# Performance work log

Hardware: AMD Instinct MI355X
Metric: run time of the kernel (lower is better)

The kernel has to match this reference:

```python
import jax, jax.numpy as jnp
import numpy as np

N = 100000   # nodes
E = 1600000  # edges (avg degree 16)
D = 64       # feature / hidden / embedding dim
OUT = 2
NEG_SLOPE = 0.2


def setup_inputs() -> dict:
    key = jax.random.key(0)
    ks = jax.random.split(key, 12)
    s = 1.0 / np.sqrt(D)
    return {
        "x": jax.random.normal(ks[0], (N, D), dtype=jnp.float32),
        "edge_index": jax.random.randint(ks[1], (2, E), 0, N, dtype=jnp.int64),
        "Wl": jax.random.normal(ks[2], (3, D, D), dtype=jnp.float32) * s,
        "bl": jnp.zeros((3, D), dtype=jnp.float32),
        "Wr": jax.random.normal(ks[3], (3, D, D), dtype=jnp.float32) * s,
        "br": jnp.zeros((3, D), dtype=jnp.float32),
        "att": jax.random.normal(ks[4], (3, D), dtype=jnp.float32) * s,
        "bg": jnp.zeros((3, D), dtype=jnp.float32),
        "Ws": jax.random.normal(ks[5], (3, D, D), dtype=jnp.float32) * s,
        "bs": jnp.zeros((3, D), dtype=jnp.float32),
        "Wout": jax.random.normal(ks[6], (D, OUT), dtype=jnp.float32) * s,
        "bout": jnp.zeros((OUT,), dtype=jnp.float32),
    }


def _gatv2(h, src, dst, Wl, bl, Wr, br, att, bg):
    # GATv2Conv (heads=1, concat, add_self_loops=False):
    #   e_ij = att . LeakyReLU(Wl h_j + Wr h_i); softmax over incoming edges of i;
    #   out_i = sum_j alpha_ij * (Wl h_j) + bias
    xl = h @ Wl + bl                      # [N, D] source transform
    xr = h @ Wr + br                      # [N, D] dest transform
    e = jax.nn.leaky_relu(xl[src] + xr[dst], NEG_SLOPE) @ att  # [E]
    m = jax.ops.segment_max(e, dst, num_segments=N)            # per-dest max
    a = jnp.exp(e - m[dst])                                    # [E]
    denom = jax.ops.segment_sum(a, dst, num_segments=N)        # [N]
    alpha = a / denom[dst]                                     # [E]
    agg = jax.ops.segment_sum(alpha[:, None] * xl[src], dst, num_segments=N)
    return agg + bg                                            # [N, D]


def reference(x, edge_index, Wl, bl, Wr, br, att, bg, Ws, bs, Wout, bout):
    src, dst = edge_index[0], edge_index[1]
    # layer 1: gat1 + skip1, relu (dropout_rate=0 -> identity)
    h = jax.nn.relu(_gatv2(x, src, dst, Wl[0], bl[0], Wr[0], br[0], att[0], bg[0])
                    + x @ Ws[0] + bs[0])
    # middle layer
    h = jax.nn.relu(_gatv2(h, src, dst, Wl[1], bl[1], Wr[1], br[1], att[1], bg[1])
                    + h @ Ws[1] + bs[1])
    # last gat layer: no relu after
    h = _gatv2(h, src, dst, Wl[2], bl[2], Wr[2], br[2], att[2], bg[2]) + h @ Ws[2] + bs[2]
    return h @ Wout + bout
```

## Files before the change

kernel.cpp:

```cpp
#include <hip/hip_runtime.h>
#include <stdint.h>

#define NN 100000
#define EE 1600000
#define DD 64
#define NBUCK 391
#define SCWG 200
#define SCCHUNK 8000

using short8 = __attribute__((ext_vector_type(8))) short;
using f32x4  = __attribute__((ext_vector_type(4))) float;
using f2     = __attribute__((ext_vector_type(2))) float;


__device__ __forceinline__ unsigned short bf16_rne(float f) {
    unsigned int u = __float_as_uint(f);
    unsigned int r = (u + 0x7FFFu + ((u >> 16) & 1u)) >> 16;
    return (unsigned short)r;
}
__device__ __forceinline__ float bf16_to_f32(unsigned short h) {
    return __uint_as_float(((unsigned int)h) << 16);
}


__global__ void bucket_hist(const int* __restrict__ dst, int* __restrict__ bhist) {
    __shared__ int h[NBUCK];
    int t = threadIdx.x;
    for (int b = t; b < NBUCK; b += 256) h[b] = 0;
    __syncthreads();
    int start = blockIdx.x * SCCHUNK;
    int endi = min(start + SCCHUNK, EE);
    for (int e = start + t; e < endi; e += 256)
        atomicAdd(&h[dst[e] >> 8], 1);
    __syncthreads();
    for (int b = t; b < NBUCK; b += 256)
        if (h[b]) atomicAdd(&bhist[b], h[b]);
}

__global__ void bucket_scan(const int* __restrict__ bhist, int* __restrict__ bbase,
                            int* __restrict__ bcursor, int* __restrict__ offsets) {
    __shared__ int s[512];
    int t = threadIdx.x;
    int v = (t < NBUCK) ? bhist[t] : 0;
    s[t] = v;
    __syncthreads();
    for (int off = 1; off < 512; off <<= 1) {
        int a = (t >= off) ? s[t - off] : 0;
        __syncthreads();
        s[t] += a;
        __syncthreads();
    }
    if (t < NBUCK) { int excl = s[t] - v; bbase[t] = excl; bcursor[t] = excl; }
    if (t == 0) { bbase[NBUCK] = EE; offsets[NN] = EE; }
}

__global__ void bucket_scatter(const int* __restrict__ src, const int* __restrict__ dst,
                               int* __restrict__ bcursor, unsigned int* __restrict__ bedges) {
    __shared__ int cnt[NBUCK];
    __shared__ int lcur[NBUCK];
    int t = threadIdx.x;
    for (int b = t; b < NBUCK; b += 256) cnt[b] = 0;
    __syncthreads();
    int start = blockIdx.x * SCCHUNK;
    int endi = min(start + SCCHUNK, EE);
    for (int e = start + t; e < endi; e += 256)
        atomicAdd(&cnt[dst[e] >> 8], 1);
    __syncthreads();
    for (int b = t; b < NBUCK; b += 256) {
        int c = cnt[b];
        lcur[b] = c ? atomicAdd(&bcursor[b], c) : 0;
    }
    __syncthreads();
    for (int e = start + t; e < endi; e += 256) {
        int d = dst[e];
        int pos = atomicAdd(&lcur[d >> 8], 1);
        bedges[pos] = ((unsigned int)(d & 255) << 24) | (unsigned int)src[e];
    }
}

__global__ void bucket_csr(const unsigned int* __restrict__ bedges, const int* __restrict__ bbase,
                           int* __restrict__ offsets, int* __restrict__ csr) {
    __shared__ int ncnt[256];
    __shared__ int lofs[256];
    int b = blockIdx.x;
    int t = threadIdx.x;
    int beg = bbase[b], endb = bbase[b + 1];
    ncnt[t] = 0;
    __syncthreads();
    for (int e = beg + t; e < endb; e += 256)
        atomicAdd(&ncnt[bedges[e] >> 24], 1);
    __syncthreads();
    int v = ncnt[t];
    lofs[t] = v;
    __syncthreads();
    for (int off = 1; off < 256; off <<= 1) {
        int a = (t >= off) ? lofs[t - off] : 0;
        __syncthreads();
        lofs[t] += a;
        __syncthreads();
    }
    int excl = lofs[t] - v;
    int node = b * 256 + t;
    if (node < NN) offsets[node] = beg + excl;
    __syncthreads();
    ncnt[t] = beg + excl;
    __syncthreads();
    for (int e = beg + t; e < endb; e += 256) {
        unsigned int ed = bedges[e];
        int pos = atomicAdd(&ncnt[ed >> 24], 1);
        csr[pos] = (int)(ed & 0xFFFFFFu);
    }
}


__global__ void conv_wx(const float* __restrict__ Wl, const float* __restrict__ Wr,
                        const float* __restrict__ Ws, const float* __restrict__ x,
                        unsigned short* __restrict__ Wt_hi, unsigned short* __restrict__ Wt_lo,
                        unsigned short* __restrict__ Ahi, unsigned short* __restrict__ Alo) {
    if (blockIdx.x < 144) {
        int e = blockIdx.x * 256 + threadIdx.x;
        if (e >= 9 * 4096) return;
        int mat = e >> 12;
        int r   = e & 4095;
        int k   = r >> 6, n = r & 63;
        int L = mat / 3, j = mat % 3;
        const float* W = (j == 0) ? Wl : ((j == 1) ? Wr : Ws);
        float v = W[L * 4096 + k * 64 + n];
        unsigned short hi = bf16_rne(v);
        unsigned short lo = bf16_rne(v - bf16_to_f32(hi));
        Wt_hi[mat * 4096 + n * 64 + k] = hi;
        Wt_lo[mat * 4096 + n * 64 + k] = lo;
    } else {
        int i = (blockIdx.x - 144) * 256 + threadIdx.x;
        int total = NN * 16;
        int stride = (gridDim.x - 144) * 256;
        for (; i < total; i += stride) {
            float4 v = *(const float4*)&x[(size_t)i * 4];
            ushort4 h, l;
            h.x = bf16_rne(v.x); l.x = bf16_rne(v.x - bf16_to_f32(h.x));
            h.y = bf16_rne(v.y); l.y = bf16_rne(v.y - bf16_to_f32(h.y));
            h.z = bf16_rne(v.z); l.z = bf16_rne(v.z - bf16_to_f32(h.z));
            h.w = bf16_rne(v.w); l.w = bf16_rne(v.w - bf16_to_f32(h.w));
            *(ushort4*)&Ahi[(size_t)i * 4] = h;
            *(ushort4*)&Alo[(size_t)i * 4] = l;
        }
    }
}


__global__ __launch_bounds__(256) void gemm_mfma(
    const unsigned short* __restrict__ Ahi, const unsigned short* __restrict__ Alo,
    const unsigned short* __restrict__ Wt_hi, const unsigned short* __restrict__ Wt_lo,
    const float* __restrict__ bl, const float* __restrict__ br, const float* __restrict__ bs,
    unsigned short* __restrict__ Xlb, float* __restrict__ XRS) {
    int lane = threadIdx.x & 63;
    int wid  = threadIdx.x >> 6;
    int m0 = (blockIdx.x * 4 + wid) * 16;
    if (m0 >= NN) return;

    int l4 = lane & 15;
    int hi = lane >> 4;
    int koff = hi * 8;

    int arow = m0 + l4;
    bool rowok = (arow < NN);
    if (!rowok) arow = NN - 1;

    const unsigned short* abase = Ahi + (size_t)arow * 64;
    const unsigned short* lbase = Alo + (size_t)arow * 64;
    short8 ahi0 = *(const short8*)(abase + koff);
    short8 ahi1 = *(const short8*)(abase + 32 + koff);
    short8 alo0 = *(const short8*)(lbase + koff);
    short8 alo1 = *(const short8*)(lbase + 32 + koff);

    int nbase0 = hi * 4;

#pragma unroll
    for (int m = 0; m < 3; m++) {
        const unsigned short* wh = Wt_hi + m * 4096;
        const unsigned short* wl = Wt_lo + m * 4096;
        const float* bias = (m == 0) ? bl : ((m == 1) ? br : bs);
#pragma unroll
        for (int tt = 0; tt < 4; tt++) {
            int ncol = tt * 16 + l4;
            const unsigned short* bh = wh + ncol * 64 + koff;
            const unsigned short* blo = wl + ncol * 64 + koff;
            short8 bhi0 = *(const short8*)bh;
            short8 bhi1 = *(const short8*)(bh + 32);
            short8 blo0 = *(const short8*)blo;
            short8 blo1 = *(const short8*)(blo + 32);

            f32x4 acc = {0.f, 0.f, 0.f, 0.f};
            acc = __builtin_amdgcn_mfma_f32_16x16x32_bf16(bhi0, ahi0, acc, 0, 0, 0);
            acc = __builtin_amdgcn_mfma_f32_16x16x32_bf16(bhi1, ahi1, acc, 0, 0, 0);
            acc = __builtin_amdgcn_mfma_f32_16x16x32_bf16(blo0, ahi0, acc, 0, 0, 0);
            acc = __builtin_amdgcn_mfma_f32_16x16x32_bf16(blo1, ahi1, acc, 0, 0, 0);
            acc = __builtin_amdgcn_mfma_f32_16x16x32_bf16(bhi0, alo0, acc, 0, 0, 0);
            acc = __builtin_amdgcn_mfma_f32_16x16x32_bf16(bhi1, alo1, acc, 0, 0, 0);

            int nb = tt * 16 + nbase0;
            float4 bb = *(const float4*)&bias[nb];
            if (rowok) {
                if (m == 0) {
                    ushort4 hh;
                    hh.x = bf16_rne(acc[0] + bb.x);
                    hh.y = bf16_rne(acc[1] + bb.y);
                    hh.z = bf16_rne(acc[2] + bb.z);
                    hh.w = bf16_rne(acc[3] + bb.w);
                    *(ushort4*)&Xlb[(size_t)arow * 64 + nb] = hh;
                } else {
                    float4 vv;
                    vv.x = acc[0] + bb.x; vv.y = acc[1] + bb.y;
                    vv.z = acc[2] + bb.z; vv.w = acc[3] + bb.w;
                    int coff = (m == 1) ? 0 : 64;
                    *(float4*)&XRS[(size_t)arow * 128 + coff + nb] = vv;
                }
            }
        }
    }
}


__device__ __forceinline__ float group_sum16(float t) {
    t += __int_as_float(__builtin_amdgcn_update_dpp(0, __float_as_int(t), 0xB1, 0xF, 0xF, true));
    t += __int_as_float(__builtin_amdgcn_update_dpp(0, __float_as_int(t), 0x4E, 0xF, 0xF, true));
    t += __int_as_float(__builtin_amdgcn_update_dpp(0, __float_as_int(t), 0x141, 0xF, 0xF, true));
    t += __int_as_float(__builtin_amdgcn_update_dpp(0, __float_as_int(t), 0x140, 0xF, 0xF, true));
    return t;
}

__global__ __launch_bounds__(256) void node_kernel(
    const unsigned short* __restrict__ Xlb, const float* __restrict__ XRS,
    const int* __restrict__ offsets, const int* __restrict__ csr,
    const float* __restrict__ att, const float* __restrict__ bg,
    unsigned short* __restrict__ houtHi, unsigned short* __restrict__ houtLo, int do_relu,
    const float* __restrict__ Wout, const float* __restrict__ bout,
    float* __restrict__ outp, int do_out) {
    int lane = threadIdx.x & 63;
    int wid  = threadIdx.x >> 6;
    int i = blockIdx.x * 4 + wid;
    if (i >= NN) return;
    int sub = lane & 15;
    int grp = lane >> 4;

    float4 xr4  = *(const float4*)&XRS[(size_t)i * 128 + sub * 4];
    float4 att4 = *(const float4*)&att[sub * 4];
    const float LOG2E = 1.44269504088896340736f;
    f2 xr01 = {xr4.x, xr4.y}, xr23 = {xr4.z, xr4.w};
    f2 at01 = {att4.x * LOG2E, att4.y * LOG2E}, at23 = {att4.z * LOG2E, att4.w * LOG2E};

    f2 agg01 = {0.f, 0.f}, agg23 = {0.f, 0.f};
    float denom = 0.f;
    int beg = offsets[i], end = offsets[i + 1];

    for (int j0 = beg; j0 < end; j0 += 8) {
        int jA = j0 + grp, jB = j0 + grp + 4;
        bool vA = jA < end, vB = jB < end;
        int sA = csr[vA ? jA : beg];
        int sB = csr[vB ? jB : beg];
        uint2 uA = *(const uint2*)&Xlb[(size_t)sA * 64 + sub * 4];
        uint2 uB = *(const uint2*)&Xlb[(size_t)sB * 64 + sub * 4];
        f2 xA01 = { __uint_as_float(uA.x << 16), __uint_as_float(uA.x & 0xFFFF0000u) };
        f2 xA23 = { __uint_as_float(uA.y << 16), __uint_as_float(uA.y & 0xFFFF0000u) };
        f2 xB01 = { __uint_as_float(uB.x << 16), __uint_as_float(uB.x & 0xFFFF0000u) };
        f2 xB23 = { __uint_as_float(uB.y << 16), __uint_as_float(uB.y & 0xFFFF0000u) };

        f2 sA01 = xA01 + xr01;
        f2 sA23 = xA23 + xr23;
        f2 sB01 = xB01 + xr01;
        f2 sB23 = xB23 + xr23;
        f2 lA01 = { fmaxf(sA01.x, 0.2f * sA01.x), fmaxf(sA01.y, 0.2f * sA01.y) };
        f2 lA23 = { fmaxf(sA23.x, 0.2f * sA23.x), fmaxf(sA23.y, 0.2f * sA23.y) };
        f2 lB01 = { fmaxf(sB01.x, 0.2f * sB01.x), fmaxf(sB01.y, 0.2f * sB01.y) };
        f2 lB23 = { fmaxf(sB23.x, 0.2f * sB23.x), fmaxf(sB23.y, 0.2f * sB23.y) };

        f2 tAv = lA01 * at01 + lA23 * at23;
        f2 tBv = lB01 * at01 + lB23 * at23;
        float tA = group_sum16(tAv.x + tAv.y);
        float tB = group_sum16(tBv.x + tBv.y);
        float aA = vA ? exp2f(tA) : 0.f;
        float aB = vB ? exp2f(tB) : 0.f;

        f2 aAv = {aA, aA};
        f2 aBv = {aB, aB};
        agg01 += aAv * xA01 + aBv * xB01;
        agg23 += aAv * xA23 + aBv * xB23;
        denom += aA + aB;
    }

    float aggx = agg01.x, aggy = agg01.y, aggz = agg23.x, aggw = agg23.y;
#pragma unroll
    for (int m = 16; m <= 32; m <<= 1) {
        aggx  += __shfl_xor(aggx, m, 64);
        aggy  += __shfl_xor(aggy, m, 64);
        aggz  += __shfl_xor(aggz, m, 64);
        aggw  += __shfl_xor(aggw, m, 64);
        denom += __shfl_xor(denom, m, 64);
    }

    float inv = (denom > 0.f) ? (1.0f / denom) : 0.f;
    float4 sk4 = *(const float4*)&XRS[(size_t)i * 128 + 64 + sub * 4];
    float4 bg4 = *(const float4*)&bg[sub * 4];
    float4 res;
    res.x = aggx * inv + bg4.x + sk4.x;
    res.y = aggy * inv + bg4.y + sk4.y;
    res.z = aggz * inv + bg4.z + sk4.z;
    res.w = aggw * inv + bg4.w + sk4.w;
    if (do_relu) {
        res.x = fmaxf(res.x, 0.f); res.y = fmaxf(res.y, 0.f);
        res.z = fmaxf(res.z, 0.f); res.w = fmaxf(res.w, 0.f);
    }
    if (do_out) {
        float4 w01 = *(const float4*)&Wout[8 * sub];
        float4 w23 = *(const float4*)&Wout[8 * sub + 4];
        float o0 = res.x * w01.x + res.y * w01.z + res.z * w23.x + res.w * w23.z;
        float o1 = res.x * w01.y + res.y * w01.w + res.z * w23.y + res.w * w23.w;
        o0 = group_sum16(o0);
        o1 = group_sum16(o1);
        if (lane == 0) {
            outp[(size_t)i * 2 + 0] = o0 + bout[0];
            outp[(size_t)i * 2 + 1] = o1 + bout[1];
        }
    } else {
        if (grp == 0) {
            ushort4 h, l;
            h.x = bf16_rne(res.x); l.x = bf16_rne(res.x - bf16_to_f32(h.x));
            h.y = bf16_rne(res.y); l.y = bf16_rne(res.y - bf16_to_f32(h.y));
            h.z = bf16_rne(res.z); l.z = bf16_rne(res.z - bf16_to_f32(h.z));
            h.w = bf16_rne(res.w); l.w = bf16_rne(res.w - bf16_to_f32(h.w));
            *(ushort4*)&houtHi[(size_t)i * 64 + sub * 4] = h;
            *(ushort4*)&houtLo[(size_t)i * 64 + sub * 4] = l;
        }
    }
}


extern "C" void kernel_launch(void* const* d_in, const int* in_sizes, int n_in,
                              void* d_out, int out_size, void* d_ws, size_t ws_size,
                              hipStream_t stream) {
    const float* x    = (const float*)d_in[0];
    const int*   ei   = (const int*)d_in[1];
    const float* Wl   = (const float*)d_in[2];
    const float* bl   = (const float*)d_in[3];
    const float* Wr   = (const float*)d_in[4];
    const float* br   = (const float*)d_in[5];
    const float* att  = (const float*)d_in[6];
    const float* bg   = (const float*)d_in[7];
    const float* Ws   = (const float*)d_in[8];
    const float* bs   = (const float*)d_in[9];
    const float* Wout = (const float*)d_in[10];
    const float* bout = (const float*)d_in[11];
    float* out = (float*)d_out;

    size_t off = 0;
    char* base = (char*)d_ws;
    auto alloc = [&](size_t bytes) -> void* {
        void* p = base + off;
        off += (bytes + 255) & ~(size_t)255;
        return p;
    };
    unsigned short* Xlb = (unsigned short*)alloc((size_t)NN * 64 * 2);
    float* XRS  = (float*)alloc((size_t)NN * 128 * 4);
    unsigned short* Ahi = (unsigned short*)alloc((size_t)NN * 64 * 2);
    unsigned short* Alo = (unsigned short*)alloc((size_t)NN * 64 * 2);
    unsigned short* Bhi = (unsigned short*)alloc((size_t)NN * 64 * 2);
    unsigned short* Blo = (unsigned short*)alloc((size_t)NN * 64 * 2);
    unsigned short* Wthi = (unsigned short*)alloc((size_t)9 * 4096 * 2);
    unsigned short* Wtlo = (unsigned short*)alloc((size_t)9 * 4096 * 2);
    int*  bhist  = (int*)alloc((size_t)NBUCK * 4);
    int*  bbase  = (int*)alloc((size_t)(NBUCK + 1) * 4);
    int*  bcur   = (int*)alloc((size_t)NBUCK * 4);
    unsigned int* bedges = (unsigned int*)alloc((size_t)EE * 4);
    int*  offs   = (int*)alloc((size_t)(NN + 1) * 4);
    int*  csr    = (int*)alloc((size_t)EE * 4);

    const int* src = ei;
    const int* dst = ei + EE;

    hipMemsetAsync(bhist, 0, (size_t)NBUCK * 4, stream);
    bucket_hist<<<SCWG, 256, 0, stream>>>(dst, bhist);
    bucket_scan<<<1, 512, 0, stream>>>(bhist, bbase, bcur, offs);
    bucket_scatter<<<SCWG, 256, 0, stream>>>(src, dst, bcur, bedges);
    bucket_csr<<<NBUCK, 256, 0, stream>>>(bedges, bbase, offs, csr);

    conv_wx<<<144 + 400, 256, 0, stream>>>(Wl, Wr, Ws, x, Wthi, Wtlo, Ahi, Alo);

    unsigned short* curHi = Ahi; unsigned short* curLo = Alo;
    unsigned short* nxtHi = Bhi; unsigned short* nxtLo = Blo;
    for (int L = 0; L < 3; L++) {
        gemm_mfma<<<(NN + 63) / 64, 256, 0, stream>>>(
            curHi, curLo, Wthi + (size_t)L * 3 * 4096, Wtlo + (size_t)L * 3 * 4096,
            bl + L * 64, br + L * 64, bs + L * 64, Xlb, XRS);
        node_kernel<<<NN / 4, 256, 0, stream>>>(
            Xlb, XRS, offs, csr, att + L * 64, bg + L * 64,
            nxtHi, nxtLo, (L < 2) ? 1 : 0,
            Wout, bout, out, (L == 2) ? 1 : 0);
        unsigned short* th = curHi; curHi = nxtHi; nxtHi = th;
        unsigned short* tl = curLo; curLo = nxtLo; nxtLo = tl;
    }
}
```

Measured before the change: 399.9 us.

## Store dest/skip transforms in bf16, unroll edge loop by four, use native exp2

```diff
diff --git a/kernel.cpp b/kernel.cpp
--- a/kernel.cpp
+++ b/kernel.cpp
@@ -20,6 +20,11 @@
 }
 __device__ __forceinline__ float bf16_to_f32(unsigned short h) {
     return __uint_as_float(((unsigned int)h) << 16);
+}
+__device__ __forceinline__ float exp2_native(float x) {
+    float r;
+    asm("v_exp_f32 %0, %1" : "=v"(r) : "v"(x));
+    return r;
 }
 
 
@@ -152,7 +157,7 @@
     const unsigned short* __restrict__ Ahi, const unsigned short* __restrict__ Alo,
     const unsigned short* __restrict__ Wt_hi, const unsigned short* __restrict__ Wt_lo,
     const float* __restrict__ bl, const float* __restrict__ br, const float* __restrict__ bs,
-    unsigned short* __restrict__ Xlb, float* __restrict__ XRS) {
+    unsigned short* __restrict__ Xlb, unsigned short* __restrict__ XRS) {
     int lane = threadIdx.x & 63;
     int wid  = threadIdx.x >> 6;
     int m0 = (blockIdx.x * 4 + wid) * 16;
@@ -201,19 +206,16 @@
             int nb = tt * 16 + nbase0;
             float4 bb = *(const float4*)&bias[nb];
             if (rowok) {
+                ushort4 hh;
+                hh.x = bf16_rne(acc[0] + bb.x);
+                hh.y = bf16_rne(acc[1] + bb.y);
+                hh.z = bf16_rne(acc[2] + bb.z);
+                hh.w = bf16_rne(acc[3] + bb.w);
                 if (m == 0) {
-                    ushort4 hh;
-                    hh.x = bf16_rne(acc[0] + bb.x);
-                    hh.y = bf16_rne(acc[1] + bb.y);
-                    hh.z = bf16_rne(acc[2] + bb.z);
-                    hh.w = bf16_rne(acc[3] + bb.w);
                     *(ushort4*)&Xlb[(size_t)arow * 64 + nb] = hh;
                 } else {
-                    float4 vv;
-                    vv.x = acc[0] + bb.x; vv.y = acc[1] + bb.y;
-                    vv.z = acc[2] + bb.z; vv.w = acc[3] + bb.w;
                     int coff = (m == 1) ? 0 : 64;
-                    *(float4*)&XRS[(size_t)arow * 128 + coff + nb] = vv;
+                    *(ushort4*)&XRS[(size_t)arow * 128 + coff + nb] = hh;
                 }
             }
         }
@@ -229,8 +231,13 @@
     return t;
 }
 
+__device__ __forceinline__ void unpack4(uint2 u, f2& v01, f2& v23) {
+    v01 = f2{ __uint_as_float(u.x << 16), __uint_as_float(u.x & 0xFFFF0000u) };
+    v23 = f2{ __uint_as_float(u.y << 16), __uint_as_float(u.y & 0xFFFF0000u) };
+}
+
 __global__ __launch_bounds__(256) void node_kernel(
-    const unsigned short* __restrict__ Xlb, const float* __restrict__ XRS,
+    const unsigned short* __restrict__ Xlb, const unsigned short* __restrict__ XRS,
     const int* __restrict__ offsets, const int* __restrict__ csr,
     const float* __restrict__ att, const float* __restrict__ bg,
     unsigned short* __restrict__ houtHi, unsigned short* __restrict__ houtLo, int do_relu,
@@ -243,49 +250,63 @@
     int sub = lane & 15;
     int grp = lane >> 4;
 
-    float4 xr4  = *(const float4*)&XRS[(size_t)i * 128 + sub * 4];
+    f2 xr01, xr23;
+    unpack4(*(const uint2*)&XRS[(size_t)i * 128 + sub * 4], xr01, xr23);
     float4 att4 = *(const float4*)&att[sub * 4];
     const float LOG2E = 1.44269504088896340736f;
-    f2 xr01 = {xr4.x, xr4.y}, xr23 = {xr4.z, xr4.w};
     f2 at01 = {att4.x * LOG2E, att4.y * LOG2E}, at23 = {att4.z * LOG2E, att4.w * LOG2E};
 
     f2 agg01 = {0.f, 0.f}, agg23 = {0.f, 0.f};
     float denom = 0.f;
     int beg = offsets[i], end = offsets[i + 1];
 
-    for (int j0 = beg; j0 < end; j0 += 8) {
-        int jA = j0 + grp, jB = j0 + grp + 4;
-        bool vA = jA < end, vB = jB < end;
+    for (int j0 = beg; j0 < end; j0 += 16) {
+        int jA = j0 + grp, jB = jA + 4, jC = jA + 8, jD = jA + 12;
+        bool vA = jA < end, vB = jB < end, vC = jC < end, vD = jD < end;
         int sA = csr[vA ? jA : beg];
         int sB = csr[vB ? jB : beg];
+        int sC = csr[vC ? jC : beg];
+        int sD = csr[vD ? jD : beg];
         uint2 uA = *(const uint2*)&Xlb[(size_t)sA * 64 + sub * 4];
         uint2 uB = *(const uint2*)&Xlb[(size_t)sB * 64 + sub * 4];
-        f2 xA01 = { __uint_as_float(uA.x << 16), __uint_as_float(uA.x & 0xFFFF0000u) };
-        f2 xA23 = { __uint_as_float(uA.y << 16), __uint_as_float(uA.y & 0xFFFF0000u) };
-        f2 xB01 = { __uint_as_float(uB.x << 16), __uint_as_float(uB.x & 0xFFFF0000u) };
-        f2 xB23 = { __uint_as_float(uB.y << 16), __uint_as_float(uB.y & 0xFFFF0000u) };
-
-        f2 sA01 = xA01 + xr01;
-        f2 sA23 = xA23 + xr23;
-        f2 sB01 = xB01 + xr01;
-        f2 sB23 = xB23 + xr23;
+        uint2 uC = *(const uint2*)&Xlb[(size_t)sC * 64 + sub * 4];
+        uint2 uD = *(const uint2*)&Xlb[(size_t)sD * 64 + sub * 4];
+        f2 xA01, xA23, xB01, xB23, xC01, xC23, xD01, xD23;
+        unpack4(uA, xA01, xA23);
+        unpack4(uB, xB01, xB23);
+        unpack4(uC, xC01, xC23);
+        unpack4(uD, xD01, xD23);
+
+        f2 sA01 = xA01 + xr01, sA23 = xA23 + xr23;
+        f2 sB01 = xB01 + xr01, sB23 = xB23 + xr23;
+        f2 sC01 = xC01 + xr01, sC23 = xC23 + xr23;
+        f2 sD01 = xD01 + xr01, sD23 = xD23 + xr23;
         f2 lA01 = { fmaxf(sA01.x, 0.2f * sA01.x), fmaxf(sA01.y, 0.2f * sA01.y) };
         f2 lA23 = { fmaxf(sA23.x, 0.2f * sA23.x), fmaxf(sA23.y, 0.2f * sA23.y) };
         f2 lB01 = { fmaxf(sB01.x, 0.2f * sB01.x), fmaxf(sB01.y, 0.2f * sB01.y) };
         f2 lB23 = { fmaxf(sB23.x, 0.2f * sB23.x), fmaxf(sB23.y, 0.2f * sB23.y) };
+        f2 lC01 = { fmaxf(sC01.x, 0.2f * sC01.x), fmaxf(sC01.y, 0.2f * sC01.y) };
+        f2 lC23 = { fmaxf(sC23.x, 0.2f * sC23.x), fmaxf(sC23.y, 0.2f * sC23.y) };
+        f2 lD01 = { fmaxf(sD01.x, 0.2f * sD01.x), fmaxf(sD01.y, 0.2f * sD01.y) };
+        f2 lD23 = { fmaxf(sD23.x, 0.2f * sD23.x), fmaxf(sD23.y, 0.2f * sD23.y) };
 
         f2 tAv = lA01 * at01 + lA23 * at23;
         f2 tBv = lB01 * at01 + lB23 * at23;
+        f2 tCv = lC01 * at01 + lC23 * at23;
+        f2 tDv = lD01 * at01 + lD23 * at23;
         float tA = group_sum16(tAv.x + tAv.y);
         float tB = group_sum16(tBv.x + tBv.y);
-        float aA = vA ? exp2f(tA) : 0.f;
-        float aB = vB ? exp2f(tB) : 0.f;
-
-        f2 aAv = {aA, aA};
-        f2 aBv = {aB, aB};
-        agg01 += aAv * xA01 + aBv * xB01;
-        agg23 += aAv * xA23 + aBv * xB23;
-        denom += aA + aB;
+        float tC = group_sum16(tCv.x + tCv.y);
+        float tD = group_sum16(tDv.x + tDv.y);
+        float aA = vA ? exp2_native(tA) : 0.f;
+        float aB = vB ? exp2_native(tB) : 0.f;
+        float aC = vC ? exp2_native(tC) : 0.f;
+        float aD = vD ? exp2_native(tD) : 0.f;
+
+        f2 aAv = {aA, aA}, aBv = {aB, aB}, aCv = {aC, aC}, aDv = {aD, aD};
+        agg01 += aAv * xA01 + aBv * xB01 + aCv * xC01 + aDv * xD01;
+        agg23 += aAv * xA23 + aBv * xB23 + aCv * xC23 + aDv * xD23;
+        denom += (aA + aB) + (aC + aD);
     }
 
     float aggx = agg01.x, aggy = agg01.y, aggz = agg23.x, aggw = agg23.y;
@@ -299,13 +320,14 @@
     }
 
     float inv = (denom > 0.f) ? (1.0f / denom) : 0.f;
-    float4 sk4 = *(const float4*)&XRS[(size_t)i * 128 + 64 + sub * 4];
+    f2 sk01, sk23;
+    unpack4(*(const uint2*)&XRS[(size_t)i * 128 + 64 + sub * 4], sk01, sk23);
     float4 bg4 = *(const float4*)&bg[sub * 4];
     float4 res;
-    res.x = aggx * inv + bg4.x + sk4.x;
-    res.y = aggy * inv + bg4.y + sk4.y;
-    res.z = aggz * inv + bg4.z + sk4.z;
-    res.w = aggw * inv + bg4.w + sk4.w;
+    res.x = aggx * inv + bg4.x + sk01.x;
+    res.y = aggy * inv + bg4.y + sk01.y;
+    res.z = aggz * inv + bg4.z + sk23.x;
+    res.w = aggw * inv + bg4.w + sk23.y;
     if (do_relu) {
         res.x = fmaxf(res.x, 0.f); res.y = fmaxf(res.y, 0.f);
         res.z = fmaxf(res.z, 0.f); res.w = fmaxf(res.w, 0.f);
@@ -360,7 +382,7 @@
         return p;
     };
     unsigned short* Xlb = (unsigned short*)alloc((size_t)NN * 64 * 2);
-    float* XRS  = (float*)alloc((size_t)NN * 128 * 4);
+    unsigned short* XRS = (unsigned short*)alloc((size_t)NN * 128 * 2);
     unsigned short* Ahi = (unsigned short*)alloc((size_t)NN * 64 * 2);
     unsigned short* Alo = (unsigned short*)alloc((size_t)NN * 64 * 2);
     unsigned short* Bhi = (unsigned short*)alloc((size_t)NN * 64 * 2);
```

Measured after the change: 401.7 us. About the same (+0.4%).

## Store dest/skip transforms as bf16 and compute 32 rows per GEMM wave

Applied to the files above, without the earlier changes.

```diff
diff --git a/kernel.cpp b/kernel.cpp
--- a/kernel.cpp
+++ b/kernel.cpp
@@ -152,26 +152,33 @@
     const unsigned short* __restrict__ Ahi, const unsigned short* __restrict__ Alo,
     const unsigned short* __restrict__ Wt_hi, const unsigned short* __restrict__ Wt_lo,
     const float* __restrict__ bl, const float* __restrict__ br, const float* __restrict__ bs,
-    unsigned short* __restrict__ Xlb, float* __restrict__ XRS) {
+    unsigned short* __restrict__ Xlb, unsigned short* __restrict__ XRS) {
     int lane = threadIdx.x & 63;
     int wid  = threadIdx.x >> 6;
-    int m0 = (blockIdx.x * 4 + wid) * 16;
+    int m0 = (blockIdx.x * 4 + wid) * 32;
     if (m0 >= NN) return;
 
     int l4 = lane & 15;
     int hi = lane >> 4;
     int koff = hi * 8;
 
-    int arow = m0 + l4;
-    bool rowok = (arow < NN);
-    if (!rowok) arow = NN - 1;
-
-    const unsigned short* abase = Ahi + (size_t)arow * 64;
-    const unsigned short* lbase = Alo + (size_t)arow * 64;
-    short8 ahi0 = *(const short8*)(abase + koff);
-    short8 ahi1 = *(const short8*)(abase + 32 + koff);
-    short8 alo0 = *(const short8*)(lbase + koff);
-    short8 alo1 = *(const short8*)(lbase + 32 + koff);
+    int arow0 = m0 + l4, arow1 = m0 + 16 + l4;
+    bool ok0 = arow0 < NN, ok1 = arow1 < NN;
+    int ar0 = ok0 ? arow0 : NN - 1;
+    int ar1 = ok1 ? arow1 : NN - 1;
+
+    const unsigned short* ab0 = Ahi + (size_t)ar0 * 64;
+    const unsigned short* lb0 = Alo + (size_t)ar0 * 64;
+    const unsigned short* ab1 = Ahi + (size_t)ar1 * 64;
+    const unsigned short* lb1 = Alo + (size_t)ar1 * 64;
+    short8 a0hi0 = *(const short8*)(ab0 + koff);
+    short8 a0hi1 = *(const short8*)(ab0 + 32 + koff);
+    short8 a0lo0 = *(const short8*)(lb0 + koff);
+    short8 a0lo1 = *(const short8*)(lb0 + 32 + koff);
+    short8 a1hi0 = *(const short8*)(ab1 + koff);
+    short8 a1hi1 = *(const short8*)(ab1 + 32 + koff);
+    short8 a1lo0 = *(const short8*)(lb1 + koff);
+    short8 a1lo1 = *(const short8*)(lb1 + 32 + koff);
 
     int nbase0 = hi * 4;
 
@@ -190,31 +197,35 @@
             short8 blo0 = *(const short8*)blo;
             short8 blo1 = *(const short8*)(blo + 32);
 
-            f32x4 acc = {0.f, 0.f, 0.f, 0.f};
-            acc = __builtin_amdgcn_mfma_f32_16x16x32_bf16(bhi0, ahi0, acc, 0, 0, 0);
-            acc = __builtin_amdgcn_mfma_f32_16x16x32_bf16(bhi1, ahi1, acc, 0, 0, 0);
-            acc = __builtin_amdgcn_mfma_f32_16x16x32_bf16(blo0, ahi0, acc, 0, 0, 0);
-            acc = __builtin_amdgcn_mfma_f32_16x16x32_bf16(blo1, ahi1, acc, 0, 0, 0);
-            acc = __builtin_amdgcn_mfma_f32_16x16x32_bf16(bhi0, alo0, acc, 0, 0, 0);
-            acc = __builtin_amdgcn_mfma_f32_16x16x32_bf16(bhi1, alo1, acc, 0, 0, 0);
+            f32x4 acc0 = {0.f, 0.f, 0.f, 0.f};
+            f32x4 acc1 = {0.f, 0.f, 0.f, 0.f};
+            acc0 = __builtin_amdgcn_mfma_f32_16x16x32_bf16(bhi0, a0hi0, acc0, 0, 0, 0);
+            acc1 = __builtin_amdgcn_mfma_f32_16x16x32_bf16(bhi0, a1hi0, acc1, 0, 0, 0);
+            acc0 = __builtin_amdgcn_mfma_f32_16x16x32_bf16(bhi1, a0hi1, acc0, 0, 0, 0);
+            acc1 = __builtin_amdgcn_mfma_f32_16x16x32_bf16(bhi1, a1hi1, acc1, 0, 0, 0);
+            acc0 = __builtin_amdgcn_mfma_f32_16x16x32_bf16(blo0, a0hi0, acc0, 0, 0, 0);
+            acc1 = __builtin_amdgcn_mfma_f32_16x16x32_bf16(blo0, a1hi0, acc1, 0, 0, 0);
+            acc0 = __builtin_amdgcn_mfma_f32_16x16x32_bf16(blo1, a0hi1, acc0, 0, 0, 0);
+            acc1 = __builtin_amdgcn_mfma_f32_16x16x32_bf16(blo1, a1hi1, acc1, 0, 0, 0);
+            acc0 = __builtin_amdgcn_mfma_f32_16x16x32_bf16(bhi0, a0lo0, acc0, 0, 0, 0);
+            acc1 = __builtin_amdgcn_mfma_f32_16x16x32_bf16(bhi0, a1lo0, acc1, 0, 0, 0);
+            acc0 = __builtin_amdgcn_mfma_f32_16x16x32_bf16(bhi1, a0lo1, acc0, 0, 0, 0);
+            acc1 = __builtin_amdgcn_mfma_f32_16x16x32_bf16(bhi1, a1lo1, acc1, 0, 0, 0);
 
             int nb = tt * 16 + nbase0;
             float4 bb = *(const float4*)&bias[nb];
-            if (rowok) {
-                if (m == 0) {
-                    ushort4 hh;
-                    hh.x = bf16_rne(acc[0] + bb.x);
-                    hh.y = bf16_rne(acc[1] + bb.y);
-                    hh.z = bf16_rne(acc[2] + bb.z);
-                    hh.w = bf16_rne(acc[3] + bb.w);
-                    *(ushort4*)&Xlb[(size_t)arow * 64 + nb] = hh;
-                } else {
-                    float4 vv;
-                    vv.x = acc[0] + bb.x; vv.y = acc[1] + bb.y;
-                    vv.z = acc[2] + bb.z; vv.w = acc[3] + bb.w;
-                    int coff = (m == 1) ? 0 : 64;
-                    *(float4*)&XRS[(size_t)arow * 128 + coff + nb] = vv;
-                }
+            ushort4 h0, h1;
+            h0.x = bf16_rne(acc0[0] + bb.x); h0.y = bf16_rne(acc0[1] + bb.y);
+            h0.z = bf16_rne(acc0[2] + bb.z); h0.w = bf16_rne(acc0[3] + bb.w);
+            h1.x = bf16_rne(acc1[0] + bb.x); h1.y = bf16_rne(acc1[1] + bb.y);
+            h1.z = bf16_rne(acc1[2] + bb.z); h1.w = bf16_rne(acc1[3] + bb.w);
+            if (m == 0) {
+                if (ok0) *(ushort4*)&Xlb[(size_t)ar0 * 64 + nb] = h0;
+                if (ok1) *(ushort4*)&Xlb[(size_t)ar1 * 64 + nb] = h1;
+            } else {
+                int coff = (m == 1) ? 0 : 64;
+                if (ok0) *(ushort4*)&XRS[(size_t)ar0 * 128 + coff + nb] = h0;
+                if (ok1) *(ushort4*)&XRS[(size_t)ar1 * 128 + coff + nb] = h1;
             }
         }
     }
@@ -229,8 +240,13 @@
     return t;
 }
 
+__device__ __forceinline__ void unpack4(uint2 u, f2& v01, f2& v23) {
+    v01 = f2{ __uint_as_float(u.x << 16), __uint_as_float(u.x & 0xFFFF0000u) };
+    v23 = f2{ __uint_as_float(u.y << 16), __uint_as_float(u.y & 0xFFFF0000u) };
+}
+
 __global__ __launch_bounds__(256) void node_kernel(
-    const unsigned short* __restrict__ Xlb, const float* __restrict__ XRS,
+    const unsigned short* __restrict__ Xlb, const unsigned short* __restrict__ XRS,
     const int* __restrict__ offsets, const int* __restrict__ csr,
     const float* __restrict__ att, const float* __restrict__ bg,
     unsigned short* __restrict__ houtHi, unsigned short* __restrict__ houtLo, int do_relu,
@@ -243,27 +259,25 @@
     int sub = lane & 15;
     int grp = lane >> 4;
 
-    float4 xr4  = *(const float4*)&XRS[(size_t)i * 128 + sub * 4];
+    f2 xr01, xr23;
+    unpack4(*(const uint2*)&XRS[(size_t)i * 128 + sub * 4], xr01, xr23);
     float4 att4 = *(const float4*)&att[sub * 4];
-    const float LOG2E = 1.44269504088896340736f;
-    f2 xr01 = {xr4.x, xr4.y}, xr23 = {xr4.z, xr4.w};
-    f2 at01 = {att4.x * LOG2E, att4.y * LOG2E}, at23 = {att4.z * LOG2E, att4.w * LOG2E};
+    f2 at01 = {att4.x, att4.y}, at23 = {att4.z, att4.w};
 
     f2 agg01 = {0.f, 0.f}, agg23 = {0.f, 0.f};
     float denom = 0.f;
     int beg = offsets[i], end = offsets[i + 1];
 
     for (int j0 = beg; j0 < end; j0 += 8) {
-        int jA = j0 + grp, jB = j0 + grp + 4;
+        int jA = j0 + grp, jB = jA + 4;
         bool vA = jA < end, vB = jB < end;
         int sA = csr[vA ? jA : beg];
         int sB = csr[vB ? jB : beg];
         uint2 uA = *(const uint2*)&Xlb[(size_t)sA * 64 + sub * 4];
         uint2 uB = *(const uint2*)&Xlb[(size_t)sB * 64 + sub * 4];
-        f2 xA01 = { __uint_as_float(uA.x << 16), __uint_as_float(uA.x & 0xFFFF0000u) };
-        f2 xA23 = { __uint_as_float(uA.y << 16), __uint_as_float(uA.y & 0xFFFF0000u) };
-        f2 xB01 = { __uint_as_float(uB.x << 16), __uint_as_float(uB.x & 0xFFFF0000u) };
-        f2 xB23 = { __uint_as_float(uB.y << 16), __uint_as_float(uB.y & 0xFFFF0000u) };
+        f2 xA01, xA23, xB01, xB23;
+        unpack4(uA, xA01, xA23);
+        unpack4(uB, xB01, xB23);
 
         f2 sA01 = xA01 + xr01;
         f2 sA23 = xA23 + xr23;
@@ -278,8 +292,8 @@
         f2 tBv = lB01 * at01 + lB23 * at23;
         float tA = group_sum16(tAv.x + tAv.y);
         float tB = group_sum16(tBv.x + tBv.y);
-        float aA = vA ? exp2f(tA) : 0.f;
-        float aB = vB ? exp2f(tB) : 0.f;
+        float aA = vA ? __expf(tA) : 0.f;
+        float aB = vB ? __expf(tB) : 0.f;
 
         f2 aAv = {aA, aA};
         f2 aBv = {aB, aB};
@@ -299,13 +313,14 @@
     }
 
     float inv = (denom > 0.f) ? (1.0f / denom) : 0.f;
-    float4 sk4 = *(const float4*)&XRS[(size_t)i * 128 + 64 + sub * 4];
+    f2 sk01, sk23;
+    unpack4(*(const uint2*)&XRS[(size_t)i * 128 + 64 + sub * 4], sk01, sk23);
     float4 bg4 = *(const float4*)&bg[sub * 4];
     float4 res;
-    res.x = aggx * inv + bg4.x + sk4.x;
-    res.y = aggy * inv + bg4.y + sk4.y;
-    res.z = aggz * inv + bg4.z + sk4.z;
-    res.w = aggw * inv + bg4.w + sk4.w;
+    res.x = aggx * inv + bg4.x + sk01.x;
+    res.y = aggy * inv + bg4.y + sk01.y;
+    res.z = aggz * inv + bg4.z + sk23.x;
+    res.w = aggw * inv + bg4.w + sk23.y;
     if (do_relu) {
         res.x = fmaxf(res.x, 0.f); res.y = fmaxf(res.y, 0.f);
         res.z = fmaxf(res.z, 0.f); res.w = fmaxf(res.w, 0.f);
@@ -360,7 +375,7 @@
         return p;
     };
     unsigned short* Xlb = (unsigned short*)alloc((size_t)NN * 64 * 2);
-    float* XRS  = (float*)alloc((size_t)NN * 128 * 4);
+    unsigned short* XRS = (unsigned short*)alloc((size_t)NN * 128 * 2);
     unsigned short* Ahi = (unsigned short*)alloc((size_t)NN * 64 * 2);
     unsigned short* Alo = (unsigned short*)alloc((size_t)NN * 64 * 2);
     unsigned short* Bhi = (unsigned short*)alloc((size_t)NN * 64 * 2);
@@ -388,7 +403,7 @@
     unsigned short* curHi = Ahi; unsigned short* curLo = Alo;
     unsigned short* nxtHi = Bhi; unsigned short* nxtLo = Blo;
     for (int L = 0; L < 3; L++) {
-        gemm_mfma<<<(NN + 63) / 64, 256, 0, stream>>>(
+        gemm_mfma<<<(NN + 127) / 128, 256, 0, stream>>>(
             curHi, curLo, Wthi + (size_t)L * 3 * 4096, Wtlo + (size_t)L * 3 * 4096,
             bl + L * 64, br + L * 64, bs + L * 64, Xlb, XRS);
         node_kernel<<<NN / 4, 256, 0, stream>>>(
```

New measurement: 351.1 us. -12.2%, faster.
